# Kernel tuning notes

Measured on AMD Instinct MI355X. Metric: run time of the kernel, lower is better.

## Reference

```python
import jax, jax.numpy as jnp
import numpy as np

N_NODES = 50000
N_EDGES = 600000
N_GRAPHS = 500
NODES_PER_GRAPH = 100
D = 128


def gcn_conv(x, W, b, src, dst, norm, n_nodes):
    # x' = D^-1/2 (A+I) D^-1/2 (x @ W) + b   (PyG GCNConv, add_self_loops=True)
    xw = x @ W                                # [N, out]
    msg = xw[src] * norm[:, None]             # [E+N, out]
    out = jax.ops.segment_sum(msg, dst, num_segments=n_nodes)
    return out + b


def setup_inputs() -> dict:
    key = jax.random.key(0)
    ks = jax.random.split(key, 8)
    x = jax.random.normal(ks[0], (N_NODES, D), dtype=jnp.float32)
    edge_index = jax.random.randint(ks[1], (2, N_EDGES), 0, N_NODES, dtype=jnp.int64)
    # batch: 500 graphs of 100 nodes each
    batch = jnp.repeat(jnp.arange(N_GRAPHS, dtype=jnp.int64), NODES_PER_GRAPH)
    # exactly 2 neighbor nodes per graph (first two of each graph)
    pat = jnp.zeros((NODES_PER_GRAPH,), dtype=jnp.float32).at[:2].set(1.0)
    is_neighbor = jnp.tile(pat, N_GRAPHS)
    scale = 1.0 / np.sqrt(D)
    W1 = jax.random.normal(ks[2], (D, D), dtype=jnp.float32) * scale
    b1 = jnp.zeros((D,), dtype=jnp.float32)
    W2 = jax.random.normal(ks[3], (D, D), dtype=jnp.float32) * scale
    b2 = jnp.zeros((D,), dtype=jnp.float32)
    W3 = jax.random.normal(ks[4], (D, D), dtype=jnp.float32) * scale
    b3 = jnp.zeros((D,), dtype=jnp.float32)
    return {"x": x, "edge_index": edge_index, "is_neighbor": is_neighbor,
            "batch": batch, "W1": W1, "b1": b1, "W2": W2, "b2": b2,
            "W3": W3, "b3": b3}


def reference(x, edge_index, is_neighbor, batch, W1, b1, W2, b2, W3, b3):
    n = x.shape[0]
    loop = jnp.arange(n, dtype=edge_index.dtype)
    src = jnp.concatenate([edge_index[0], loop])   # self loops appended
    dst = jnp.concatenate([edge_index[1], loop])
    deg = jax.ops.segment_sum(jnp.ones_like(dst, dtype=x.dtype), dst, num_segments=n)
    dinv = jnp.where(deg > 0, jax.lax.rsqrt(deg), 0.0)
    norm = dinv[src] * dinv[dst]                   # [E+N]

    h = gcn_conv(x, W1, b1, src, dst, norm, n)
    h = jax.nn.relu(h)
    h = gcn_conv(h, W2, b2, src, dst, norm, n)
    h = jax.nn.relu(h)
    h = gcn_conv(h, W3, b3, src, dst, norm, n)

    h = h * is_neighbor[:, None]
    pooled = jax.ops.segment_sum(h, batch, num_segments=N_GRAPHS)
    return pooled / 2.0
```

## Files before the change

kernel.cpp:

```cpp
#include <hip/hip_runtime.h>
#include <hip/hip_fp16.h>
#include <type_traits>

#define D 128

typedef __attribute__((ext_vector_type(8))) _Float16 f16x8;
typedef __attribute__((ext_vector_type(4))) float f32x4;


__global__ void count_kernel(const int* __restrict__ src, const int* __restrict__ dst,
                             const float* __restrict__ is_n,
                             int* __restrict__ cnt, int* __restrict__ mark, int E) {
    int e = blockIdx.x * blockDim.x + threadIdx.x;
    if (e < E) {
        int d = dst[e];
        atomicAdd(&cnt[d], 1);
        if (is_n[d] != 0.f) mark[src[e]] = 1;
    }
}

__global__ __launch_bounds__(256) void psumB_kernel(const int* __restrict__ cnt,
                                                    const int* __restrict__ mark,
                                                    const float* __restrict__ is_n,
                                                    int* __restrict__ bsum_c,
                                                    int* __restrict__ bsum_m, int n) {
    __shared__ int s[256], s2[256];
    int t = threadIdx.x;
    int i = blockIdx.x * 256 + t;
    s[t] = (i < n) ? cnt[i] : 0;
    s2[t] = (i < n) ? (mark[i] | (is_n[i] != 0.f ? 1 : 0)) : 0;
    __syncthreads();
    for (int off = 128; off > 0; off >>= 1) {
        if (t < off) { s[t] += s[t + off]; s2[t] += s2[t + off]; }
        __syncthreads();
    }
    if (t == 0) { bsum_c[blockIdx.x] = s[0]; bsum_m[blockIdx.x] = s2[0]; }
}

__global__ __launch_bounds__(256) void bscanB_kernel(const int* __restrict__ bsum_c,
                                                     const int* __restrict__ bsum_m,
                                                     int* __restrict__ boff_c,
                                                     int* __restrict__ boff_m,
                                                     int* __restrict__ na, int PB) {
    __shared__ int s[256];
    int t = threadIdx.x;
    int v = (t < PB) ? bsum_c[t] : 0;
    s[t] = v;
    __syncthreads();
    for (int off = 1; off < 256; off <<= 1) {
        int add = (t >= off) ? s[t - off] : 0;
        __syncthreads();
        s[t] += add;
        __syncthreads();
    }
    if (t < PB) boff_c[t] = s[t] - v;
    __syncthreads();
    int v2 = (t < PB) ? bsum_m[t] : 0;
    s[t] = v2;
    __syncthreads();
    for (int off = 1; off < 256; off <<= 1) {
        int add = (t >= off) ? s[t - off] : 0;
        __syncthreads();
        s[t] += add;
        __syncthreads();
    }
    if (t < PB) boff_m[t] = s[t] - v2;
    if (t == PB - 1) na[0] = s[t];
}

__global__ __launch_bounds__(256) void finB_kernel(const int* __restrict__ cnt,
                                                   const int* __restrict__ mark,
                                                   const float* __restrict__ is_n,
                                                   const int* __restrict__ boff_c,
                                                   const int* __restrict__ boff_m,
                                                   int* __restrict__ rowstart,
                                                   int* __restrict__ cursor,
                                                   float* __restrict__ dinv,
                                                   int* __restrict__ act, int n, int E) {
    __shared__ int s[256];
    int t = threadIdx.x;
    int i = blockIdx.x * 256 + t;
    int c = (i < n) ? cnt[i] : 0;
    s[t] = c;
    __syncthreads();
    for (int off = 1; off < 256; off <<= 1) {
        int add = (t >= off) ? s[t - off] : 0;
        __syncthreads();
        s[t] += add;
        __syncthreads();
    }
    if (i < n) {
        int excl = s[t] - c + boff_c[blockIdx.x];
        rowstart[i] = excl;
        cursor[i] = excl;
        dinv[i] = rsqrtf(1.0f + (float)c);
    }
    if (i == 0) rowstart[n] = E;
    __syncthreads();
    int m = (i < n) ? (mark[i] | (is_n[i] != 0.f ? 1 : 0)) : 0;
    s[t] = m;
    __syncthreads();
    for (int off = 1; off < 256; off <<= 1) {
        int add = (t >= off) ? s[t - off] : 0;
        __syncthreads();
        s[t] += add;
        __syncthreads();
    }
    if (m) act[s[t] - 1 + boff_m[blockIdx.x]] = i;
}

__global__ void fill_kernel(const int* __restrict__ src, const int* __restrict__ dst,
                            int* __restrict__ cursor, int* __restrict__ csr_src, int E) {
    int e = blockIdx.x * blockDim.x + threadIdx.x;
    if (e < E) {
        int d = dst[e];
        int pos = atomicAdd(&cursor[d], 1);
        csr_src[pos] = src[e];
    }
}


__global__ __launch_bounds__(256) void packw_kernel(const float* __restrict__ W1,
                                                    const float* __restrict__ W2,
                                                    const float* __restrict__ W3,
                                                    __half* __restrict__ Wp) {
    int gid = blockIdx.x * 256 + threadIdx.x;
    int m = gid >> 11;
    int idx = gid & 2047;
    const float* W = (m == 0) ? W1 : (m == 1) ? W2 : W3;
    int l = idx & 63;
    int nt = (idx >> 6) & 7;
    int ks = idx >> 9;
    int kb = ks * 32 + (l >> 4) * 8;
    int col = nt * 16 + (l & 15);
    __half tmp[8];
#pragma unroll
    for (int j = 0; j < 8; j++) tmp[j] = __float2half(W[(kb + j) * D + col]);
    *(float4*)&Wp[(size_t)gid * 8] = *(float4*)tmp;
}


template <typename AT>
__global__ __launch_bounds__(256, 2) void gemm_mfma_kernel(const AT* __restrict__ X,
                                                           const __half* __restrict__ Wp,
                                                           const float* __restrict__ dinv,
                                                           __half* __restrict__ Y, int M) {
    int lane = threadIdx.x & 63;
    int wid = threadIdx.x >> 6;
    f16x8 bf[4][8];
    {
        const float4* wp = (const float4*)Wp;
#pragma unroll
        for (int ks = 0; ks < 4; ks++)
#pragma unroll
            for (int nt = 0; nt < 8; nt++) {
                float4 t = wp[(ks * 8 + nt) * 64 + lane];
                bf[ks][nt] = *(f16x8*)&t;
            }
    }
    int row_l = lane & 15;
    int kgrp = lane >> 4;
    int tiles = M >> 4;
    int nw = gridDim.x * 4;
    for (int tile = blockIdx.x * 4 + wid; tile < tiles; tile += nw) {
        int row0 = tile << 4;
        const AT* ap = X + (size_t)(row0 + row_l) * D + kgrp * 8;
        f32x4 acc[8];
#pragma unroll
        for (int nt = 0; nt < 8; nt++) acc[nt] = (f32x4){0.f, 0.f, 0.f, 0.f};
#pragma unroll
        for (int ks = 0; ks < 4; ks++) {
            f16x8 a;
            if constexpr (std::is_same<AT, float>::value) {
                float4 a0 = *(const float4*)(ap + ks * 32);
                float4 a1 = *(const float4*)(ap + ks * 32 + 4);
                a[0] = (_Float16)a0.x; a[1] = (_Float16)a0.y;
                a[2] = (_Float16)a0.z; a[3] = (_Float16)a0.w;
                a[4] = (_Float16)a1.x; a[5] = (_Float16)a1.y;
                a[6] = (_Float16)a1.z; a[7] = (_Float16)a1.w;
            } else {
                float4 t = *(const float4*)(const void*)(ap + ks * 32);
                a = *(f16x8*)&t;
            }
#pragma unroll
            for (int nt = 0; nt < 8; nt++)
                acc[nt] = __builtin_amdgcn_mfma_f32_16x16x32_f16(a, bf[ks][nt],
                                                                 acc[nt], 0, 0, 0);
        }
        float ds[4];
#pragma unroll
        for (int r = 0; r < 4; r++) ds[r] = dinv[row0 + kgrp * 4 + r];
        __half* yb = Y + (size_t)row0 * D;
#pragma unroll
        for (int nt = 0; nt < 8; nt++)
#pragma unroll
            for (int r = 0; r < 4; r++)
                yb[(size_t)(kgrp * 4 + r) * D + nt * 16 + row_l] =
                    __float2half(ds[r] * acc[nt][r]);
    }
}


__device__ __forceinline__ void acc_row8(float acc[8], const __half* __restrict__ row,
                                         int l16) {
    float4 r = ((const float4*)row)[l16];
    const __half2* h2 = (const __half2*)&r;
#pragma unroll
    for (int k = 0; k < 4; k++) {
        float2 f = __half22float2(h2[k]);
        acc[2 * k]     += f.x;
        acc[2 * k + 1] += f.y;
    }
}

__device__ __forceinline__ void gather_node(const __half* __restrict__ XWs,
                                            const int* __restrict__ rowstart,
                                            const int* __restrict__ csr_src,
                                            int v, int g, int l16, float acc[8]) {
#pragma unroll
    for (int k = 0; k < 8; k++) acc[k] = 0.f;
    int e0 = rowstart[v];
    int deg = rowstart[v + 1] - e0;
    int j = g;
    for (; j + 4 < deg; j += 8) {
        int u0 = csr_src[e0 + j];
        int u1 = csr_src[e0 + j + 4];
        acc_row8(acc, XWs + (size_t)u0 * D, l16);
        acc_row8(acc, XWs + (size_t)u1 * D, l16);
    }
    if (j < deg) acc_row8(acc, XWs + (size_t)csr_src[e0 + j] * D, l16);
#pragma unroll
    for (int k = 0; k < 8; k++) acc[k] += __shfl_xor(acc[k], 16);
#pragma unroll
    for (int k = 0; k < 8; k++) acc[k] += __shfl_xor(acc[k], 32);
    acc_row8(acc, XWs + (size_t)v * D, l16);
}


__global__ __launch_bounds__(256) void agg_gemm_kernel(const __half* __restrict__ XWs,
                                                       const float* __restrict__ bias,
                                                       const float* __restrict__ dinv,
                                                       const int* __restrict__ rowstart,
                                                       const int* __restrict__ csr_src,
                                                       const __half* __restrict__ Wp2,
                                                       __half* __restrict__ Y) {
    __shared__ __half hs[16][136];
    int t = threadIdx.x;
    int wid = t >> 6, lane = t & 63;
    int g = lane >> 4, l16 = lane & 15;
    int block0 = blockIdx.x * 16;
    f16x8 bf[4][2];
    {
        const float4* wp = (const float4*)Wp2;
#pragma unroll
        for (int ks = 0; ks < 4; ks++)
#pragma unroll
            for (int j = 0; j < 2; j++) {
                float4 tmp = wp[(ks * 8 + wid * 2 + j) * 64 + lane];
                bf[ks][j] = *(f16x8*)&tmp;
            }
    }
    float4 b0 = ((const float4*)bias)[l16 * 2];
    float4 b1 = ((const float4*)bias)[l16 * 2 + 1];
#pragma unroll
    for (int i = 0; i < 4; i++) {
        int v = block0 + wid * 4 + i;
        float acc[8];
        gather_node(XWs, rowstart, csr_src, v, g, l16, acc);
        float dv = dinv[v];
        __half o[8];
        o[0] = __float2half(fmaxf(b0.x + dv * acc[0], 0.f));
        o[1] = __float2half(fmaxf(b0.y + dv * acc[1], 0.f));
        o[2] = __float2half(fmaxf(b0.z + dv * acc[2], 0.f));
        o[3] = __float2half(fmaxf(b0.w + dv * acc[3], 0.f));
        o[4] = __float2half(fmaxf(b1.x + dv * acc[4], 0.f));
        o[5] = __float2half(fmaxf(b1.y + dv * acc[5], 0.f));
        o[6] = __float2half(fmaxf(b1.z + dv * acc[6], 0.f));
        o[7] = __float2half(fmaxf(b1.w + dv * acc[7], 0.f));
        if (g == 0) *(float4*)&hs[wid * 4 + i][l16 * 8] = *(float4*)o;
    }
    __syncthreads();
    int row_l = l16, kgrp = g;
    f32x4 acc2[2];
    acc2[0] = (f32x4){0.f, 0.f, 0.f, 0.f};
    acc2[1] = (f32x4){0.f, 0.f, 0.f, 0.f};
#pragma unroll
    for (int ks = 0; ks < 4; ks++) {
        f16x8 a = *(f16x8*)&hs[row_l][ks * 32 + kgrp * 8];
#pragma unroll
        for (int j = 0; j < 2; j++)
            acc2[j] = __builtin_amdgcn_mfma_f32_16x16x32_f16(a, bf[ks][j],
                                                             acc2[j], 0, 0, 0);
    }
    float ds[4];
#pragma unroll
    for (int r = 0; r < 4; r++) ds[r] = dinv[block0 + kgrp * 4 + r];
    __half* yb = Y + (size_t)block0 * D;
#pragma unroll
    for (int j = 0; j < 2; j++)
#pragma unroll
        for (int r = 0; r < 4; r++)
            yb[(size_t)(kgrp * 4 + r) * D + (wid * 2 + j) * 16 + row_l] =
                __float2half(ds[r] * acc2[j][r]);
}


__global__ __launch_bounds__(256) void agg_act_kernel(const __half* __restrict__ XWs,
                                                      const float* __restrict__ bias,
                                                      const float* __restrict__ dinv,
                                                      const int* __restrict__ rowstart,
                                                      const int* __restrict__ csr_src,
                                                      const int* __restrict__ act,
                                                      const int* __restrict__ na_p,
                                                      __half* __restrict__ out) {
    int wid = threadIdx.x >> 6;
    int lane = threadIdx.x & 63;
    int g = lane >> 4, l16 = lane & 15;
    int na = na_p[0];
    int stride = gridDim.x * 4;
    float4 b0 = ((const float4*)bias)[l16 * 2];
    float4 b1 = ((const float4*)bias)[l16 * 2 + 1];
    for (int i = blockIdx.x * 4 + wid; i < na; i += stride) {
        int v = act[i];
        float acc[8];
        gather_node(XWs, rowstart, csr_src, v, g, l16, acc);
        float dv = dinv[v];
        if (g == 0) {
            __half o[8];
            o[0] = __float2half(dv * fmaxf(b0.x + dv * acc[0], 0.f));
            o[1] = __float2half(dv * fmaxf(b0.y + dv * acc[1], 0.f));
            o[2] = __float2half(dv * fmaxf(b0.z + dv * acc[2], 0.f));
            o[3] = __float2half(dv * fmaxf(b0.w + dv * acc[3], 0.f));
            o[4] = __float2half(dv * fmaxf(b1.x + dv * acc[4], 0.f));
            o[5] = __float2half(dv * fmaxf(b1.y + dv * acc[5], 0.f));
            o[6] = __float2half(dv * fmaxf(b1.z + dv * acc[6], 0.f));
            o[7] = __float2half(dv * fmaxf(b1.w + dv * acc[7], 0.f));
            *(float4*)&out[(size_t)v * D + l16 * 8] = *(float4*)o;
        }
    }
}


__global__ __launch_bounds__(256) void agg_pool_kernel(const __half* __restrict__ Hs,
                                                       const float* __restrict__ dinv,
                                                       const int* __restrict__ rowstart,
                                                       const int* __restrict__ csr_src,
                                                       const float* __restrict__ is_n,
                                                       const int* __restrict__ batch,
                                                       float* __restrict__ P,
                                                       float* __restrict__ cg, int n) {
    int wid = threadIdx.x >> 6;
    int lane = threadIdx.x & 63;
    int g = lane >> 4, l16 = lane & 15;
    int v = blockIdx.x * 4 + wid;
    if (v >= n) return;
    float w_is = is_n[v];
    if (w_is == 0.f) return;
    float acc[8];
    gather_node(Hs, rowstart, csr_src, v, g, l16, acc);
    float s = w_is * dinv[v];
    int gr = batch[v];
    if (g == 0) {
        float* pb = &P[(size_t)gr * D + l16 * 8];
#pragma unroll
        for (int k = 0; k < 8; k++) atomicAdd(&pb[k], s * acc[k]);
    }
    if (lane == 0) atomicAdd(&cg[gr], w_is);
}

__global__ __launch_bounds__(64) void pool_gemm_kernel(const float* __restrict__ P,
                                                       const float* __restrict__ cg,
                                                       const float* __restrict__ W,
                                                       const float* __restrict__ b,
                                                       float* __restrict__ out, int G) {
    int g = blockIdx.x;
    if (g >= G) return;
    int c = threadIdx.x * 2;
    float2 acc = {0.f, 0.f};
    const float* pr = &P[(size_t)g * D];
#pragma unroll 4
    for (int k = 0; k < D; k++) {
        float pk = pr[k];
        float2 w = *(const float2*)&W[k * D + c];
        acc.x += pk * w.x;
        acc.y += pk * w.y;
    }
    float s = 0.5f * cg[g];
    float2 bb = *(const float2*)&b[c];
    out[(size_t)g * D + c]     = 0.5f * acc.x + s * bb.x;
    out[(size_t)g * D + c + 1] = 0.5f * acc.y + s * bb.y;
}


extern "C" void kernel_launch(void* const* d_in, const int* in_sizes, int n_in,
                              void* d_out, int out_size, void* d_ws, size_t ws_size,
                              hipStream_t stream) {
    const float* x     = (const float*)d_in[0];
    const int*   edge  = (const int*)d_in[1];
    const float* is_n  = (const float*)d_in[2];
    const int*   batch = (const int*)d_in[3];
    const float* W1 = (const float*)d_in[4];
    const float* b1 = (const float*)d_in[5];
    const float* W2 = (const float*)d_in[6];
    const float* b2 = (const float*)d_in[7];
    const float* W3 = (const float*)d_in[8];
    const float* b3 = (const float*)d_in[9];
    float* out = (float*)d_out;

    int n = in_sizes[0] / D;
    int E = in_sizes[1] / 2;
    int G = out_size / D;
    const int* esrc = edge;
    const int* edst = edge + E;

    char* p = (char*)d_ws;
    __half* xw = (__half*)p;     p += (size_t)n * D * sizeof(float);
    __half* h  = (__half*)p;     p += (size_t)n * D * sizeof(float);
    float* dinv = (float*)p;     p += (size_t)n * sizeof(float);
    int* rowstart = (int*)p;     p += (size_t)(n + 1) * sizeof(int);
    int* cursor = (int*)p;       p += (size_t)n * sizeof(int);
    int* csr_src = (int*)p;      p += (size_t)E * sizeof(int);
    int* bsum_c = (int*)p;       p += 256 * sizeof(int);
    int* bsum_m = (int*)p;       p += 256 * sizeof(int);
    int* boff_c = (int*)p;       p += 256 * sizeof(int);
    int* boff_m = (int*)p;       p += 256 * sizeof(int);
    int* act = (int*)p;          p += (size_t)n * sizeof(int);
    int* na = (int*)p;           p += 4 * sizeof(int);
    __half* Wp = (__half*)p;     p += (size_t)3 * D * D * sizeof(__half);
    int* cnt = (int*)p;          p += (size_t)n * sizeof(int);
    int* mark = (int*)p;         p += (size_t)n * sizeof(int);
    float* P = (float*)p;        p += (size_t)G * D * sizeof(float);
    float* cg = (float*)p;       p += (size_t)G * sizeof(float);
    size_t zbytes = (size_t)(2 * n) * sizeof(int) + (size_t)(G * D + G) * sizeof(float);

    int PB = (n + 255) / 256;

    hipMemsetAsync(cnt, 0, zbytes, stream);
    packw_kernel<<<24, 256, 0, stream>>>(W1, W2, W3, Wp);
    count_kernel<<<(E + 255) / 256, 256, 0, stream>>>(esrc, edst, is_n, cnt, mark, E);
    psumB_kernel<<<PB, 256, 0, stream>>>(cnt, mark, is_n, bsum_c, bsum_m, n);
    bscanB_kernel<<<1, 256, 0, stream>>>(bsum_c, bsum_m, boff_c, boff_m, na, PB);
    finB_kernel<<<PB, 256, 0, stream>>>(cnt, mark, is_n, boff_c, boff_m,
                                        rowstart, cursor, dinv, act, n, E);
    fill_kernel<<<(E + 255) / 256, 256, 0, stream>>>(esrc, edst, cursor, csr_src, E);

    gemm_mfma_kernel<float><<<512, 256, 0, stream>>>(x, Wp, dinv, xw, n);
    agg_gemm_kernel<<<n / 16, 256, 0, stream>>>(xw, b1, dinv, rowstart, csr_src,
                                                Wp + D * D, h);
    agg_act_kernel<<<1024, 256, 0, stream>>>(h, b2, dinv, rowstart, csr_src, act, na, xw);
    agg_pool_kernel<<<(n + 3) / 4, 256, 0, stream>>>(xw, dinv, rowstart, csr_src,
                                                     is_n, batch, P, cg, n);
    pool_gemm_kernel<<<G, 64, 0, stream>>>(P, cg, W3, b3, out, G);
}
```

Baseline: 174.3 us.

## Map one node per 16-lane group in aggregation kernels instead of one per wave

The gather work is remapped so each 16-lane quarter-wave handles a whole node serially, replacing the old scheme in which four lane groups split one node's edges and then combined partial sums with cross-lane shuffles. This removes the shuffle reductions and the idle three-quarters of lanes in the epilogue and atomic stages, and makes all lanes write outputs. The tradeoff is that a node's neighbor loads now form one longer serial dependency chain per group, and degree imbalance between groups in a wave causes divergence. The pool kernel's grid changes to n/16, which assumes n is a multiple of 16, and it now skips a whole wave only when no node in it is flagged.

```diff
diff --git a/kernel.cpp b/kernel.cpp
--- a/kernel.cpp
+++ b/kernel.cpp
@@ -201,9 +201,9 @@
 }
 
 
-__device__ __forceinline__ void acc_row8(float acc[8], const __half* __restrict__ row,
-                                         int l16) {
-    float4 r = ((const float4*)row)[l16];
+__device__ __forceinline__ void add_row(float acc[8], const __half* __restrict__ XWs,
+                                        int u, int l16) {
+    float4 r = ((const float4*)(XWs + (size_t)u * D))[l16];
     const __half2* h2 = (const __half2*)&r;
 #pragma unroll
     for (int k = 0; k < 4; k++) {
@@ -213,27 +213,30 @@
     }
 }
 
-__device__ __forceinline__ void gather_node(const __half* __restrict__ XWs,
-                                            const int* __restrict__ rowstart,
-                                            const int* __restrict__ csr_src,
-                                            int v, int g, int l16, float acc[8]) {
+__device__ __forceinline__ void gather_grp(const __half* __restrict__ XWs,
+                                           const int* __restrict__ csr_src,
+                                           int v, int e0, int e1, int l16,
+                                           float acc[8]) {
 #pragma unroll
     for (int k = 0; k < 8; k++) acc[k] = 0.f;
-    int e0 = rowstart[v];
-    int deg = rowstart[v + 1] - e0;
-    int j = g;
-    for (; j + 4 < deg; j += 8) {
-        int u0 = csr_src[e0 + j];
-        int u1 = csr_src[e0 + j + 4];
-        acc_row8(acc, XWs + (size_t)u0 * D, l16);
-        acc_row8(acc, XWs + (size_t)u1 * D, l16);
-    }
-    if (j < deg) acc_row8(acc, XWs + (size_t)csr_src[e0 + j] * D, l16);
-#pragma unroll
-    for (int k = 0; k < 8; k++) acc[k] += __shfl_xor(acc[k], 16);
-#pragma unroll
-    for (int k = 0; k < 8; k++) acc[k] += __shfl_xor(acc[k], 32);
-    acc_row8(acc, XWs + (size_t)v * D, l16);
+    int j = e0;
+    for (; j + 1 < e1; j += 2) {
+        int u0 = csr_src[j];
+        int u1 = csr_src[j + 1];
+        float4 r0 = ((const float4*)(XWs + (size_t)u0 * D))[l16];
+        float4 r1 = ((const float4*)(XWs + (size_t)u1 * D))[l16];
+        const __half2* a0 = (const __half2*)&r0;
+        const __half2* a1 = (const __half2*)&r1;
+#pragma unroll
+        for (int k = 0; k < 4; k++) {
+            float2 f0 = __half22float2(a0[k]);
+            float2 f1 = __half22float2(a1[k]);
+            acc[2 * k]     += f0.x + f1.x;
+            acc[2 * k + 1] += f0.y + f1.y;
+        }
+    }
+    if (j < e1) add_row(acc, XWs, csr_src[j], l16);
+    add_row(acc, XWs, v, l16);
 }
 
 
@@ -249,6 +252,23 @@
     int wid = t >> 6, lane = t & 63;
     int g = lane >> 4, l16 = lane & 15;
     int block0 = blockIdx.x * 16;
+    int v = block0 + wid * 4 + g;
+    int e0 = rowstart[v], e1 = rowstart[v + 1];
+    float acc[8];
+    gather_grp(XWs, csr_src, v, e0, e1, l16, acc);
+    float dv = dinv[v];
+    float4 b0 = ((const float4*)bias)[l16 * 2];
+    float4 b1 = ((const float4*)bias)[l16 * 2 + 1];
+    __half o[8];
+    o[0] = __float2half(fmaxf(b0.x + dv * acc[0], 0.f));
+    o[1] = __float2half(fmaxf(b0.y + dv * acc[1], 0.f));
+    o[2] = __float2half(fmaxf(b0.z + dv * acc[2], 0.f));
+    o[3] = __float2half(fmaxf(b0.w + dv * acc[3], 0.f));
+    o[4] = __float2half(fmaxf(b1.x + dv * acc[4], 0.f));
+    o[5] = __float2half(fmaxf(b1.y + dv * acc[5], 0.f));
+    o[6] = __float2half(fmaxf(b1.z + dv * acc[6], 0.f));
+    o[7] = __float2half(fmaxf(b1.w + dv * acc[7], 0.f));
+    *(float4*)&hs[wid * 4 + g][l16 * 8] = *(float4*)o;
     f16x8 bf[4][2];
     {
         const float4* wp = (const float4*)Wp2;
@@ -259,25 +279,6 @@
                 float4 tmp = wp[(ks * 8 + wid * 2 + j) * 64 + lane];
                 bf[ks][j] = *(f16x8*)&tmp;
             }
-    }
-    float4 b0 = ((const float4*)bias)[l16 * 2];
-    float4 b1 = ((const float4*)bias)[l16 * 2 + 1];
-#pragma unroll
-    for (int i = 0; i < 4; i++) {
-        int v = block0 + wid * 4 + i;
-        float acc[8];
-        gather_node(XWs, rowstart, csr_src, v, g, l16, acc);
-        float dv = dinv[v];
-        __half o[8];
-        o[0] = __float2half(fmaxf(b0.x + dv * acc[0], 0.f));
-        o[1] = __float2half(fmaxf(b0.y + dv * acc[1], 0.f));
-        o[2] = __float2half(fmaxf(b0.z + dv * acc[2], 0.f));
-        o[3] = __float2half(fmaxf(b0.w + dv * acc[3], 0.f));
-        o[4] = __float2half(fmaxf(b1.x + dv * acc[4], 0.f));
-        o[5] = __float2half(fmaxf(b1.y + dv * acc[5], 0.f));
-        o[6] = __float2half(fmaxf(b1.z + dv * acc[6], 0.f));
-        o[7] = __float2half(fmaxf(b1.w + dv * acc[7], 0.f));
-        if (g == 0) *(float4*)&hs[wid * 4 + i][l16 * 8] = *(float4*)o;
     }
     __syncthreads();
     int row_l = l16, kgrp = g;
@@ -313,30 +314,29 @@
                                                       const int* __restrict__ act,
                                                       const int* __restrict__ na_p,
                                                       __half* __restrict__ out) {
-    int wid = threadIdx.x >> 6;
-    int lane = threadIdx.x & 63;
+    int t = threadIdx.x;
+    int wid = t >> 6, lane = t & 63;
     int g = lane >> 4, l16 = lane & 15;
     int na = na_p[0];
-    int stride = gridDim.x * 4;
+    int stride = gridDim.x * 16;
     float4 b0 = ((const float4*)bias)[l16 * 2];
     float4 b1 = ((const float4*)bias)[l16 * 2 + 1];
-    for (int i = blockIdx.x * 4 + wid; i < na; i += stride) {
+    for (int i = blockIdx.x * 16 + wid * 4 + g; i < na; i += stride) {
         int v = act[i];
+        int e0 = rowstart[v], e1 = rowstart[v + 1];
         float acc[8];
-        gather_node(XWs, rowstart, csr_src, v, g, l16, acc);
+        gather_grp(XWs, csr_src, v, e0, e1, l16, acc);
         float dv = dinv[v];
-        if (g == 0) {
-            __half o[8];
-            o[0] = __float2half(dv * fmaxf(b0.x + dv * acc[0], 0.f));
-            o[1] = __float2half(dv * fmaxf(b0.y + dv * acc[1], 0.f));
-            o[2] = __float2half(dv * fmaxf(b0.z + dv * acc[2], 0.f));
-            o[3] = __float2half(dv * fmaxf(b0.w + dv * acc[3], 0.f));
-            o[4] = __float2half(dv * fmaxf(b1.x + dv * acc[4], 0.f));
-            o[5] = __float2half(dv * fmaxf(b1.y + dv * acc[5], 0.f));
-            o[6] = __float2half(dv * fmaxf(b1.z + dv * acc[6], 0.f));
-            o[7] = __float2half(dv * fmaxf(b1.w + dv * acc[7], 0.f));
-            *(float4*)&out[(size_t)v * D + l16 * 8] = *(float4*)o;
-        }
+        __half o[8];
+        o[0] = __float2half(dv * fmaxf(b0.x + dv * acc[0], 0.f));
+        o[1] = __float2half(dv * fmaxf(b0.y + dv * acc[1], 0.f));
+        o[2] = __float2half(dv * fmaxf(b0.z + dv * acc[2], 0.f));
+        o[3] = __float2half(dv * fmaxf(b0.w + dv * acc[3], 0.f));
+        o[4] = __float2half(dv * fmaxf(b1.x + dv * acc[4], 0.f));
+        o[5] = __float2half(dv * fmaxf(b1.y + dv * acc[5], 0.f));
+        o[6] = __float2half(dv * fmaxf(b1.z + dv * acc[6], 0.f));
+        o[7] = __float2half(dv * fmaxf(b1.w + dv * acc[7], 0.f));
+        *(float4*)&out[(size_t)v * D + l16 * 8] = *(float4*)o;
     }
 }
 
@@ -349,23 +349,23 @@
                                                        const int* __restrict__ batch,
                                                        float* __restrict__ P,
                                                        float* __restrict__ cg, int n) {
-    int wid = threadIdx.x >> 6;
-    int lane = threadIdx.x & 63;
+    int t = threadIdx.x;
+    int wid = t >> 6, lane = t & 63;
     int g = lane >> 4, l16 = lane & 15;
-    int v = blockIdx.x * 4 + wid;
-    if (v >= n) return;
+    int v = blockIdx.x * 16 + wid * 4 + g;
     float w_is = is_n[v];
-    if (w_is == 0.f) return;
-    float acc[8];
-    gather_node(Hs, rowstart, csr_src, v, g, l16, acc);
-    float s = w_is * dinv[v];
-    int gr = batch[v];
-    if (g == 0) {
+    if (__ballot(w_is != 0.f) == 0ULL) return;
+    if (w_is != 0.f) {
+        int e0 = rowstart[v], e1 = rowstart[v + 1];
+        float acc[8];
+        gather_grp(Hs, csr_src, v, e0, e1, l16, acc);
+        float s = w_is * dinv[v];
+        int gr = batch[v];
         float* pb = &P[(size_t)gr * D + l16 * 8];
 #pragma unroll
         for (int k = 0; k < 8; k++) atomicAdd(&pb[k], s * acc[k]);
-    }
-    if (lane == 0) atomicAdd(&cg[gr], w_is);
+        if (l16 == 0) atomicAdd(&cg[gr], w_is);
+    }
 }
 
 __global__ __launch_bounds__(64) void pool_gemm_kernel(const float* __restrict__ P,
@@ -448,7 +448,7 @@
     agg_gemm_kernel<<<n / 16, 256, 0, stream>>>(xw, b1, dinv, rowstart, csr_src,
                                                 Wp + D * D, h);
     agg_act_kernel<<<1024, 256, 0, stream>>>(h, b2, dinv, rowstart, csr_src, act, na, xw);
-    agg_pool_kernel<<<(n + 3) / 4, 256, 0, stream>>>(xw, dinv, rowstart, csr_src,
-                                                     is_n, batch, P, cg, n);
+    agg_pool_kernel<<<n / 16, 256, 0, stream>>>(xw, dinv, rowstart, csr_src,
+                                                is_n, batch, P, cg, n);
     pool_gemm_kernel<<<G, 64, 0, stream>>>(P, cg, W3, b3, out, G);
 }
```

Result: faster. 167.1 us (-4.1%).
